# Kernel optimization log

Hardware: AMD Instinct MI355X
Metric: run time of the kernel (lower is better)

## Reference

```python
import jax, jax.numpy as jnp
import numpy as np

B, RATIO, IN_CH, H = 32, 32, 64, 8
E = IN_CH * H                 # embed_dim = in_channels * n_heads = 512
NODES_PER_GRAPH = 512
N = B * NODES_PER_GRAPH       # 16384 source nodes


def setup_inputs() -> dict:
    key = jax.random.key(0)
    ks = jax.random.split(key, 6)
    x = jax.random.normal(ks[0], (N, E), dtype=jnp.float32)
    # edge_index is accepted by forward but unused in 'attn' mode
    edge_index = jax.random.randint(ks[1], (2, 262144), 0, N, dtype=jnp.int32)
    # per-node graph id, sorted, equal-size graphs (batch[-1] + 1 == B)
    batch = jnp.repeat(jnp.arange(B, dtype=jnp.int32), NODES_PER_GRAPH)
    # learned params: cluster query seeds + MultiheadAttention in/out projections
    xcent_base = jax.random.normal(ks[2], (RATIO, E), dtype=jnp.float32)
    in_proj_w = jax.random.normal(ks[3], (3 * E, E), dtype=jnp.float32) / np.sqrt(E).astype(np.float32)
    in_proj_b = jnp.zeros((3 * E,), dtype=jnp.float32)
    out_proj_w = jax.random.normal(ks[4], (E, E), dtype=jnp.float32) / np.sqrt(E).astype(np.float32)
    out_proj_b = jnp.zeros((E,), dtype=jnp.float32)
    return dict(x=x, edge_index=edge_index, batch=batch, xcent_base=xcent_base,
                in_proj_w=in_proj_w, in_proj_b=in_proj_b,
                out_proj_w=out_proj_w, out_proj_b=out_proj_b)


def reference(x, edge_index, batch, xcent_base, in_proj_w, in_proj_b, out_proj_w, out_proj_b):
    # BipartPool.forward, mode='attn':
    #   x_aggrs = xcent_base.repeat(batch_size, 1)  -> queries [L, E], L = B*ratio
    #   MultiheadAttention(q=x_aggrs, k=v=x, attn_mask=mask[batch].T)
    # mask[batch].T is True (disallowed) where query's graph != node's graph.
    L = B * RATIO
    head_dim = E // H
    x_aggrs = jnp.tile(xcent_base, (B, 1))                        # [L, E]

    wq, wk, wv = jnp.split(in_proj_w, 3, axis=0)                  # each [E, E]
    bq, bk, bv = jnp.split(in_proj_b, 3, axis=0)
    q = (x_aggrs @ wq.T + bq).reshape(L, H, head_dim).transpose(1, 0, 2)  # [H, L, hd]
    k = (x @ wk.T + bk).reshape(N, H, head_dim).transpose(1, 0, 2)        # [H, N, hd]
    v = (x @ wv.T + bv).reshape(N, H, head_dim).transpose(1, 0, 2)        # [H, N, hd]

    batchcent = jnp.repeat(jnp.arange(B, dtype=batch.dtype), RATIO)       # [L]
    allowed = batchcent[:, None] == batch[None, :]                        # [L, N]

    scale = np.float32(1.0 / np.sqrt(head_dim))
    scores = jnp.einsum('hld,hnd->hln', q, k) * scale                     # [H, L, N]
    scores = jnp.where(allowed[None], scores, -jnp.inf)
    attn = jax.nn.softmax(scores, axis=-1)
    out = jnp.einsum('hln,hnd->hld', attn, v)                             # [H, L, hd]
    out = out.transpose(1, 0, 2).reshape(L, E)
    xcent = out @ out_proj_w.T + out_proj_b                               # [L, E]
    # original returns (xcent.reshape(B, ratio, E), None, None, batchcent, None, None)
    return xcent.reshape(B, RATIO, E), batchcent
```

## Files before the change

### kernel.cpp

```cpp
#include <hip/hip_runtime.h>
#include <hip/hip_bf16.h>

#define NGRAPH 32
#define NHEAD 8
#define EMB 512
#define NNODES 16384
#define NPG 512
#define LQ 1024
#define PST 520

typedef __attribute__((ext_vector_type(8))) short short8;
typedef __attribute__((ext_vector_type(4))) float f32x4;

static __device__ __forceinline__ unsigned short f2bf(float f) {
  union { float f; unsigned u; } v; v.f = f;
  unsigned r = (v.u + 0x7fffu + ((v.u >> 16) & 1u)) >> 16;
  return (unsigned short)r;
}

static __device__ __forceinline__ void gload_lds16(const ushort* g, ushort* l) {
  __builtin_amdgcn_global_load_lds(
      (const __attribute__((address_space(1))) unsigned*)g,
      (__attribute__((address_space(3))) unsigned*)l, 16, 0, 0);
}

#define BARRIER_LGKM()                                        \
  do {                                                        \
    asm volatile("s_waitcnt lgkmcnt(0)" ::: "memory");        \
    __builtin_amdgcn_s_barrier();                             \
  } while (0)

__global__ void prep_x(const float* __restrict__ x, ushort* __restrict__ xb,
                       ushort* __restrict__ xbT) {
  __shared__ ushort tile[32][33];
  int bc = blockIdx.x;
  int br = blockIdx.y;
  int t = threadIdx.x, lr = t >> 5, lc = t & 31;
#pragma unroll
  for (int p = 0; p < 4; ++p) {
    int r = lr + p * 8;
    long gi = (long)(br * 32 + r) * EMB + bc * 32 + lc;
    ushort b = f2bf(x[gi]);
    xb[gi] = b;
    tile[r][lc] = b;
  }
  __syncthreads();
#pragma unroll
  for (int p = 0; p < 4; ++p) {
    int r = lr + p * 8;
    xbT[(long)(bc * 32 + r) * NNODES + br * 32 + lc] = tile[lc][r];
  }
}

__global__ void prep_w(const float* __restrict__ wv, const float* __restrict__ wo,
                       const float* __restrict__ wq, const float* __restrict__ xc,
                       ushort* __restrict__ wvb, ushort* __restrict__ wob,
                       ushort* __restrict__ wqb, ushort* __restrict__ xcb,
                       float* __restrict__ bcent) {
  int b = blockIdx.x;
  if (b == 784) {
    int i = threadIdx.x;
#pragma unroll
    for (int p = 0; p < 4; ++p) bcent[i + p * 256] = (float)((i + p * 256) >> 5);
    return;
  }
  const float* src; ushort* dst; int off;
  if (b < 256)       { src = wv; dst = wvb; off = b; }
  else if (b < 512)  { src = wo; dst = wob; off = b - 256; }
  else if (b < 768)  { src = wq; dst = wqb; off = b - 512; }
  else               { src = xc; dst = xcb; off = b - 768; }
  int i = (off * 256 + threadIdx.x) * 4;
  float4 v = *reinterpret_cast<const float4*>(src + i);
  ushort4 o;
  o.x = f2bf(v.x); o.y = f2bf(v.y); o.z = f2bf(v.z); o.w = f2bf(v.w);
  *reinterpret_cast<ushort4*>(dst + i) = o;
}

__global__ void prep_wkT(const float* __restrict__ wk, ushort* __restrict__ wkT) {
  __shared__ ushort tile[32][33];
  int bd = blockIdx.x, bk = blockIdx.y;
  int t = threadIdx.x, lr = t >> 5, lc = t & 31;
#pragma unroll
  for (int p = 0; p < 4; ++p) {
    int r = lr + p * 8;
    tile[r][lc] = f2bf(0.125f * wk[(long)(bd * 32 + r) * EMB + bk * 32 + lc]);
  }
  __syncthreads();
#pragma unroll
  for (int p = 0; p < 4; ++p) {
    int r = lr + p * 8;
    wkT[(long)(bk * 32 + r) * EMB + bd * 32 + lc] = tile[lc][r];
  }
}

__global__ __launch_bounds__(256) void qpc_mfma(
    const ushort* __restrict__ xcb, const ushort* __restrict__ wqb,
    const float* __restrict__ bq, const ushort* __restrict__ wkTb,
    ushort* __restrict__ PCb) {
  __shared__ ushort Qs[32][72];
  int h = blockIdx.x >> 2, qs = blockIdx.x & 3;
  int t = threadIdx.x, w = t >> 6, lane = t & 63;
  int lr = lane & 15, grp = lane >> 4, ko = grp * 8;

  f32x4 qa[2];
  qa[0] = (f32x4)(0.0f); qa[1] = (f32x4)(0.0f);
#pragma unroll 4
  for (int kk = 0; kk < EMB; kk += 32) {
    short8 a0 = *reinterpret_cast<const short8*>(xcb + lr * EMB + kk + ko);
    short8 a1 = *reinterpret_cast<const short8*>(xcb + (16 + lr) * EMB + kk + ko);
    short8 b  = *reinterpret_cast<const short8*>(wqb + (long)(h * 64 + w * 16 + lr) * EMB + kk + ko);
    qa[0] = __builtin_amdgcn_mfma_f32_16x16x32_bf16(a0, b, qa[0], 0, 0, 0);
    qa[1] = __builtin_amdgcn_mfma_f32_16x16x32_bf16(a1, b, qa[1], 0, 0, 0);
  }
  float bias = bq[h * 64 + w * 16 + lr];
#pragma unroll
  for (int i = 0; i < 2; ++i)
#pragma unroll
    for (int r = 0; r < 4; ++r)
      Qs[i * 16 + grp * 4 + r][w * 16 + lr] = f2bf(qa[i][r] + bias);
  __syncthreads();

  f32x4 pa[2][2];
#pragma unroll
  for (int i = 0; i < 2; ++i)
#pragma unroll
    for (int j = 0; j < 2; ++j) pa[i][j] = (f32x4)(0.0f);
#pragma unroll
  for (int kk = 0; kk < 64; kk += 32) {
    short8 a0 = *reinterpret_cast<const short8*>(&Qs[lr][kk + ko]);
    short8 a1 = *reinterpret_cast<const short8*>(&Qs[16 + lr][kk + ko]);
#pragma unroll
    for (int j = 0; j < 2; ++j) {
      short8 b = *reinterpret_cast<const short8*>(
          wkTb + (long)(qs * 128 + w * 32 + j * 16 + lr) * EMB + h * 64 + kk + ko);
      pa[0][j] = __builtin_amdgcn_mfma_f32_16x16x32_bf16(a0, b, pa[0][j], 0, 0, 0);
      pa[1][j] = __builtin_amdgcn_mfma_f32_16x16x32_bf16(a1, b, pa[1][j], 0, 0, 0);
    }
  }
#pragma unroll
  for (int i = 0; i < 2; ++i)
#pragma unroll
    for (int j = 0; j < 2; ++j)
#pragma unroll
      for (int r = 0; r < 4; ++r)
        PCb[(long)(h * 32 + i * 16 + grp * 4 + r) * EMB + qs * 128 + w * 32 + j * 16 + lr] =
            f2bf(pa[i][j][r]);
}

__global__ __launch_bounds__(512, 2) void fused_attn(
    const ushort* __restrict__ PCb, const ushort* __restrict__ xb,
    const ushort* __restrict__ xbT, const ushort* __restrict__ wvb,
    const float* __restrict__ bvb, ushort* __restrict__ aout) {
  __shared__ ushort PCl[32 * PST];
  __shared__ ushort PBuf[32 * PST];
  __shared__ ushort Bbuf[2][16384];
  __shared__ float rmax[32][8];
  __shared__ float rsum[32][8];

  const int g = blockIdx.x & 31, h = blockIdx.x >> 5;
  const int t = threadIdx.x, w = t >> 6, lane = t & 63;
  const int lr = lane & 15, grp = lane >> 4;
  const int koU = grp * 8;

  const ushort* xg  = xb  + (long)g * NPG * EMB;
  const ushort* xTg = xbT + g * NPG;

  const int srow0 = w * 64 + (lane >> 2);
  const int spart = lane & 3;

  auto STAGE1 = [&](int c, int db) {
#pragma unroll
    for (int q = 0; q < 4; ++q) {
      int row = srow0 + q * 16;
      int psrc = spart ^ ((row >> 1) & 3);
      gload_lds16(xg + (long)row * EMB + c * 32 + psrc * 8,
                  &Bbuf[db][(w * 64 + q * 16) * 32]);
    }
  };
  auto STAGE3 = [&](int c, int db) {
#pragma unroll
    for (int q = 0; q < 4; ++q) {
      int row = srow0 + q * 16;
      int psrc = spart ^ ((row >> 1) & 3);
      gload_lds16(xTg + (long)row * NNODES + c * 32 + psrc * 8,
                  &Bbuf[db][(w * 64 + q * 16) * 32]);
    }
  };

  STAGE1(0, 0);
  STAGE1(1, 1);
  {
    const ushort* pc = PCb + h * 32 * EMB;
#pragma unroll
    for (int p = 0; p < 4; ++p) {
      int u = t + p * 512;
      int row = u >> 6, col = (u & 63) * 8;
      *reinterpret_cast<short8*>(&PCl[row * PST + col]) =
          *reinterpret_cast<const short8*>(pc + row * EMB + col);
    }
  }
  BARRIER_LGKM();

  f32x4 acc[2][4];
#pragma unroll
  for (int i = 0; i < 2; ++i)
#pragma unroll
    for (int j = 0; j < 4; ++j) acc[i][j] = (f32x4)(0.0f);

#pragma unroll
  for (int c = 0; c < 16; ++c) {
    const int db = c & 1;
    asm volatile("s_waitcnt vmcnt(4)" ::: "memory");
    __builtin_amdgcn_sched_barrier(0);
    short8 a0 = *reinterpret_cast<const short8*>(&PCl[lr * PST + c * 32 + koU]);
    short8 a1 = *reinterpret_cast<const short8*>(&PCl[(16 + lr) * PST + c * 32 + koU]);
    short8 bv[4];
#pragma unroll
    for (int j = 0; j < 4; ++j) {
      int n = w * 64 + j * 16 + lr;
      int psrc = grp ^ ((n >> 1) & 3);
      bv[j] = *reinterpret_cast<const short8*>(&Bbuf[db][n * 32 + psrc * 8]);
    }
#pragma unroll
    for (int j = 0; j < 4; ++j) {
      acc[0][j] = __builtin_amdgcn_mfma_f32_16x16x32_bf16(a0, bv[j], acc[0][j], 0, 0, 0);
      acc[1][j] = __builtin_amdgcn_mfma_f32_16x16x32_bf16(a1, bv[j], acc[1][j], 0, 0, 0);
    }
    __builtin_amdgcn_sched_barrier(0);
    if (c < 14) STAGE1(c + 2, db);
    else        STAGE3(c - 14, db);
  }

#pragma unroll
  for (int i = 0; i < 2; ++i)
#pragma unroll
    for (int r = 0; r < 4; ++r) {
      float m = fmaxf(fmaxf(acc[i][0][r], acc[i][1][r]), fmaxf(acc[i][2][r], acc[i][3][r]));
      m = fmaxf(m, __shfl_xor(m, 1)); m = fmaxf(m, __shfl_xor(m, 2));
      m = fmaxf(m, __shfl_xor(m, 4)); m = fmaxf(m, __shfl_xor(m, 8));
      if (lr == 0) rmax[i * 16 + grp * 4 + r][w] = m;
    }
  BARRIER_LGKM();
#pragma unroll
  for (int i = 0; i < 2; ++i)
#pragma unroll
    for (int r = 0; r < 4; ++r) {
      int row = i * 16 + grp * 4 + r;
      float m = rmax[row][0];
#pragma unroll
      for (int q = 1; q < 8; ++q) m = fmaxf(m, rmax[row][q]);
      float s = 0.f;
#pragma unroll
      for (int j = 0; j < 4; ++j) {
        float e = __expf(acc[i][j][r] - m);
        acc[i][j][r] = e;
        s += e;
      }
      s += __shfl_xor(s, 1); s += __shfl_xor(s, 2);
      s += __shfl_xor(s, 4); s += __shfl_xor(s, 8);
      if (lr == 0) rsum[row][w] = s;
    }
  BARRIER_LGKM();
#pragma unroll
  for (int i = 0; i < 2; ++i)
#pragma unroll
    for (int r = 0; r < 4; ++r) {
      int row = i * 16 + grp * 4 + r;
      float tot = rsum[row][0];
#pragma unroll
      for (int q = 1; q < 8; ++q) tot += rsum[row][q];
      float inv = 1.f / tot;
#pragma unroll
      for (int j = 0; j < 4; ++j)
        PBuf[row * PST + w * 64 + j * 16 + lr] = f2bf(acc[i][j][r] * inv);
    }
  BARRIER_LGKM();

  f32x4 acc2[2][4];
#pragma unroll
  for (int i = 0; i < 2; ++i)
#pragma unroll
    for (int j = 0; j < 4; ++j) acc2[i][j] = (f32x4)(0.0f);

#pragma unroll
  for (int c = 0; c < 16; ++c) {
    const int db = c & 1;
    if (c < 15) asm volatile("s_waitcnt vmcnt(4)" ::: "memory");
    else        asm volatile("s_waitcnt vmcnt(0)" ::: "memory");
    __builtin_amdgcn_sched_barrier(0);
    short8 a0 = *reinterpret_cast<const short8*>(&PBuf[lr * PST + c * 32 + koU]);
    short8 a1 = *reinterpret_cast<const short8*>(&PBuf[(16 + lr) * PST + c * 32 + koU]);
    short8 bv[4];
#pragma unroll
    for (int j = 0; j < 4; ++j) {
      int e = w * 64 + j * 16 + lr;
      int psrc = grp ^ ((e >> 1) & 3);
      bv[j] = *reinterpret_cast<const short8*>(&Bbuf[db][e * 32 + psrc * 8]);
    }
#pragma unroll
    for (int j = 0; j < 4; ++j) {
      acc2[0][j] = __builtin_amdgcn_mfma_f32_16x16x32_bf16(a0, bv[j], acc2[0][j], 0, 0, 0);
      acc2[1][j] = __builtin_amdgcn_mfma_f32_16x16x32_bf16(a1, bv[j], acc2[1][j], 0, 0, 0);
    }
    __builtin_amdgcn_sched_barrier(0);
    if (c < 14) STAGE3(c + 2, db);
  }
  BARRIER_LGKM();

#pragma unroll
  for (int i = 0; i < 2; ++i)
#pragma unroll
    for (int r = 0; r < 4; ++r) {
      int row = i * 16 + grp * 4 + r;
#pragma unroll
      for (int j = 0; j < 4; ++j)
        PBuf[row * PST + w * 64 + j * 16 + lr] = f2bf(acc2[i][j][r]);
    }
  BARRIER_LGKM();

  int wr = w >> 2, wc = w & 3;
  f32x4 acc3 = (f32x4)(0.0f);
  const ushort* wvh = wvb + (long)(h * 64 + wc * 16) * EMB;
#pragma unroll
  for (int c = 0; c < 16; ++c) {
    short8 a = *reinterpret_cast<const short8*>(&PBuf[(wr * 16 + lr) * PST + c * 32 + koU]);
    short8 b = *reinterpret_cast<const short8*>(wvh + (long)lr * EMB + c * 32 + koU);
    acc3 = __builtin_amdgcn_mfma_f32_16x16x32_bf16(a, b, acc3, 0, 0, 0);
  }
  float bias = bvb[h * 64 + wc * 16 + lr];
#pragma unroll
  for (int r = 0; r < 4; ++r) {
    int row = wr * 16 + grp * 4 + r;
    aout[(long)(g * 32 + row) * EMB + h * 64 + wc * 16 + lr] = f2bf(acc3[r] + bias);
  }
}

template <int KK, int FM, int FN, int WM, int WN, bool OUT_BF16, bool HAS_BIAS>
__global__ void gemm_abt(const ushort* __restrict__ A, const ushort* __restrict__ Bm,
                         void* __restrict__ C, const float* __restrict__ bias,
                         int lda, int ldb, int ldc) {
  int tid = threadIdx.x;
  int wave = tid >> 6, lane = tid & 63;
  int wr = wave / WN, wc = wave % WN;
  int rowBase = blockIdx.y * (WM * FM * 16) + wr * FM * 16;
  int colBase = blockIdx.x * (WN * FN * 16) + wc * FN * 16;
  int lr = lane & 15;
  int ko = (lane >> 4) * 8;

  f32x4 acc[FM][FN];
#pragma unroll
  for (int i = 0; i < FM; ++i)
#pragma unroll
    for (int j = 0; j < FN; ++j) acc[i][j] = (f32x4)(0.0f);

#pragma unroll 4
  for (int kk = 0; kk < KK; kk += 32) {
    short8 av[FM], bv[FN];
#pragma unroll
    for (int i = 0; i < FM; ++i)
      av[i] = *reinterpret_cast<const short8*>(A + (long)(rowBase + i * 16 + lr) * lda + kk + ko);
#pragma unroll
    for (int j = 0; j < FN; ++j)
      bv[j] = *reinterpret_cast<const short8*>(Bm + (long)(colBase + j * 16 + lr) * ldb + kk + ko);
#pragma unroll
    for (int i = 0; i < FM; ++i)
#pragma unroll
      for (int j = 0; j < FN; ++j)
        acc[i][j] = __builtin_amdgcn_mfma_f32_16x16x32_bf16(av[i], bv[j], acc[i][j], 0, 0, 0);
  }

  int or0 = (lane >> 4) * 4;
#pragma unroll
  for (int i = 0; i < FM; ++i) {
#pragma unroll
    for (int j = 0; j < FN; ++j) {
      int col = colBase + j * 16 + lr;
      float bval = HAS_BIAS ? bias[col] : 0.f;
#pragma unroll
      for (int r = 0; r < 4; ++r) {
        int row = rowBase + i * 16 + or0 + r;
        float v = acc[i][j][r] + bval;
        if (OUT_BF16)
          ((ushort*)C)[(long)row * ldc + col] = f2bf(v);
        else
          ((float*)C)[(long)row * ldc + col] = v;
      }
    }
  }
}

extern "C" void kernel_launch(void* const* d_in, const int* in_sizes, int n_in,
                              void* d_out, int out_size, void* d_ws, size_t ws_size,
                              hipStream_t stream) {
  const float* x          = (const float*)d_in[0];
  const float* xcent_base = (const float*)d_in[3];
  const float* in_proj_w  = (const float*)d_in[4];
  const float* in_proj_b  = (const float*)d_in[5];
  const float* out_proj_w = (const float*)d_in[6];
  const float* out_proj_b = (const float*)d_in[7];

  char* w = (char*)d_ws;
  ushort* xb   = (ushort*)(w);
  ushort* xbT  = (ushort*)(w + 16777216);
  ushort* PCb  = (ushort*)(w + 33554432);
  ushort* wvb  = (ushort*)(w + 33816576);
  ushort* wob  = (ushort*)(w + 34340864);
  ushort* wqb  = (ushort*)(w + 34865152);
  ushort* wkTb = (ushort*)(w + 35389440);
  ushort* xcb  = (ushort*)(w + 35913728);
  ushort* aout = (ushort*)(w + 35946496);

  const float* wq = in_proj_w;
  const float* wk = in_proj_w + 512 * 512;
  const float* wv = in_proj_w + 1024 * 512;
  const float* bq = in_proj_b;
  const float* bv = in_proj_b + 1024;

  prep_x<<<dim3(EMB / 32, NNODES / 32), 256, 0, stream>>>(x, xb, xbT);
  prep_w<<<785, 256, 0, stream>>>(wv, out_proj_w, wq, xcent_base,
                                  wvb, wob, wqb, xcb, (float*)d_out + LQ * EMB);
  prep_wkT<<<dim3(16, 16), 256, 0, stream>>>(wk, wkTb);
  qpc_mfma<<<32, 256, 0, stream>>>(xcb, wqb, bq, wkTb, PCb);

  fused_attn<<<256, 512, 0, stream>>>(PCb, xb, xbT, wvb, bv, aout);

  gemm_abt<512, 1, 2, 2, 2, false, true><<<dim3(8, 32, 1), 256, 0, stream>>>(
      aout, wob, d_out, out_proj_b, 512, 512, 512);
}
```

Baseline: 65.60 us.

## Widen attention blocks to 1024 threads, vectorize x prep, merge weight prep kernels

```diff
diff --git a/kernel.cpp b/kernel.cpp
--- a/kernel.cpp
+++ b/kernel.cpp
@@ -30,38 +30,69 @@
     __builtin_amdgcn_s_barrier();                             \
   } while (0)
 
-__global__ void prep_x(const float* __restrict__ x, ushort* __restrict__ xb,
-                       ushort* __restrict__ xbT) {
+__global__ __launch_bounds__(256) void prep_x(const float* __restrict__ x,
+                                              ushort* __restrict__ xb,
+                                              ushort* __restrict__ xbT) {
+  __shared__ ushort tile[64][68];
+  int id = blockIdx.x;
+  int xr = id & 7, j = id >> 3;
+  int m = j >> 6, r = j & 63;
+  int g = xr + 8 * m;
+  int bc = r & 7;
+  int br = g * 8 + (r >> 3);
+  int t = threadIdx.x;
+  int trr = t >> 4, tc = t & 15;
+#pragma unroll
+  for (int p = 0; p < 4; ++p) {
+    int n = trr + p * 16;
+    long gi = (long)(br * 64 + n) * EMB + bc * 64 + tc * 4;
+    float4 v = *reinterpret_cast<const float4*>(x + gi);
+    ushort4 o;
+    o.x = f2bf(v.x); o.y = f2bf(v.y); o.z = f2bf(v.z); o.w = f2bf(v.w);
+    *reinterpret_cast<ushort4*>(xb + gi) = o;
+    *reinterpret_cast<ushort4*>(&tile[n][tc * 4]) = o;
+  }
+  __syncthreads();
+#pragma unroll
+  for (int p = 0; p < 4; ++p) {
+    int e = trr + p * 16;
+    int n0 = tc * 4;
+    ushort4 o;
+    o.x = tile[n0][e]; o.y = tile[n0 + 1][e];
+    o.z = tile[n0 + 2][e]; o.w = tile[n0 + 3][e];
+    *reinterpret_cast<ushort4*>(xbT + (long)(bc * 64 + e) * NNODES + br * 64 + n0) = o;
+  }
+}
+
+__global__ void prep_wb(const float* __restrict__ wv, const float* __restrict__ wo,
+                        const float* __restrict__ wq, const float* __restrict__ xc,
+                        const float* __restrict__ wk,
+                        ushort* __restrict__ wvb, ushort* __restrict__ wob,
+                        ushort* __restrict__ wqb, ushort* __restrict__ xcb,
+                        ushort* __restrict__ wkT, float* __restrict__ bcent) {
   __shared__ ushort tile[32][33];
-  int bc = blockIdx.x;
-  int br = blockIdx.y;
-  int t = threadIdx.x, lr = t >> 5, lc = t & 31;
-#pragma unroll
-  for (int p = 0; p < 4; ++p) {
-    int r = lr + p * 8;
-    long gi = (long)(br * 32 + r) * EMB + bc * 32 + lc;
-    ushort b = f2bf(x[gi]);
-    xb[gi] = b;
-    tile[r][lc] = b;
-  }
-  __syncthreads();
-#pragma unroll
-  for (int p = 0; p < 4; ++p) {
-    int r = lr + p * 8;
-    xbT[(long)(bc * 32 + r) * NNODES + br * 32 + lc] = tile[lc][r];
-  }
-}
-
-__global__ void prep_w(const float* __restrict__ wv, const float* __restrict__ wo,
-                       const float* __restrict__ wq, const float* __restrict__ xc,
-                       ushort* __restrict__ wvb, ushort* __restrict__ wob,
-                       ushort* __restrict__ wqb, ushort* __restrict__ xcb,
-                       float* __restrict__ bcent) {
   int b = blockIdx.x;
   if (b == 784) {
     int i = threadIdx.x;
 #pragma unroll
     for (int p = 0; p < 4; ++p) bcent[i + p * 256] = (float)((i + p * 256) >> 5);
+    return;
+  }
+  if (b >= 785) {
+    int b2 = b - 785;
+    int bd = b2 >> 4, bk = b2 & 15;
+    int t = threadIdx.x, lr = t >> 5, lc = t & 31;
+#pragma unroll
+    for (int p = 0; p < 4; ++p) {
+      int rr = lr + p * 8;
+      tile[rr][lc] = f2bf(0.125f * wk[(long)(bd * 32 + rr) * EMB + bk * 32 + lc]);
+    }
+    __syncthreads();
+#pragma unroll
+    for (int p = 0; p < 4; ++p) {
+      int rr = lr + p * 8;
+      wkT[(long)(bk * 32 + rr) * EMB + bd * 32 + lc] = tile[lc][rr];
+    }
     return;
   }
   const float* src; ushort* dst; int off;
@@ -76,23 +107,6 @@
   *reinterpret_cast<ushort4*>(dst + i) = o;
 }
 
-__global__ void prep_wkT(const float* __restrict__ wk, ushort* __restrict__ wkT) {
-  __shared__ ushort tile[32][33];
-  int bd = blockIdx.x, bk = blockIdx.y;
-  int t = threadIdx.x, lr = t >> 5, lc = t & 31;
-#pragma unroll
-  for (int p = 0; p < 4; ++p) {
-    int r = lr + p * 8;
-    tile[r][lc] = f2bf(0.125f * wk[(long)(bd * 32 + r) * EMB + bk * 32 + lc]);
-  }
-  __syncthreads();
-#pragma unroll
-  for (int p = 0; p < 4; ++p) {
-    int r = lr + p * 8;
-    wkT[(long)(bk * 32 + r) * EMB + bd * 32 + lc] = tile[lc][r];
-  }
-}
-
 __global__ __launch_bounds__(256) void qpc_mfma(
     const ushort* __restrict__ xcb, const ushort* __restrict__ wqb,
     const float* __restrict__ bq, const ushort* __restrict__ wkTb,
@@ -147,15 +161,15 @@
             f2bf(pa[i][j][r]);
 }
 
-__global__ __launch_bounds__(512, 2) void fused_attn(
+__global__ __launch_bounds__(1024) void fused_attn(
     const ushort* __restrict__ PCb, const ushort* __restrict__ xb,
     const ushort* __restrict__ xbT, const ushort* __restrict__ wvb,
     const float* __restrict__ bvb, ushort* __restrict__ aout) {
   __shared__ ushort PCl[32 * PST];
   __shared__ ushort PBuf[32 * PST];
   __shared__ ushort Bbuf[2][16384];
-  __shared__ float rmax[32][8];
-  __shared__ float rsum[32][8];
+  __shared__ float rmax[32][16];
+  __shared__ float rsum[32][16];
 
   const int g = blockIdx.x & 31, h = blockIdx.x >> 5;
   const int t = threadIdx.x, w = t >> 6, lane = t & 63;
@@ -165,25 +179,25 @@
   const ushort* xg  = xb  + (long)g * NPG * EMB;
   const ushort* xTg = xbT + g * NPG;
 
-  const int srow0 = w * 64 + (lane >> 2);
+  const int srow0 = w * 32 + (lane >> 2);
   const int spart = lane & 3;
 
   auto STAGE1 = [&](int c, int db) {
 #pragma unroll
-    for (int q = 0; q < 4; ++q) {
+    for (int q = 0; q < 2; ++q) {
       int row = srow0 + q * 16;
       int psrc = spart ^ ((row >> 1) & 3);
       gload_lds16(xg + (long)row * EMB + c * 32 + psrc * 8,
-                  &Bbuf[db][(w * 64 + q * 16) * 32]);
+                  &Bbuf[db][(w * 32 + q * 16) * 32]);
     }
   };
   auto STAGE3 = [&](int c, int db) {
 #pragma unroll
-    for (int q = 0; q < 4; ++q) {
+    for (int q = 0; q < 2; ++q) {
       int row = srow0 + q * 16;
       int psrc = spart ^ ((row >> 1) & 3);
       gload_lds16(xTg + (long)row * NNODES + c * 32 + psrc * 8,
-                  &Bbuf[db][(w * 64 + q * 16) * 32]);
+                  &Bbuf[db][(w * 32 + q * 16) * 32]);
     }
   };
 
@@ -192,8 +206,8 @@
   {
     const ushort* pc = PCb + h * 32 * EMB;
 #pragma unroll
-    for (int p = 0; p < 4; ++p) {
-      int u = t + p * 512;
+    for (int p = 0; p < 2; ++p) {
+      int u = t + p * 1024;
       int row = u >> 6, col = (u & 63) * 8;
       *reinterpret_cast<short8*>(&PCl[row * PST + col]) =
           *reinterpret_cast<const short8*>(pc + row * EMB + col);
@@ -201,28 +215,28 @@
   }
   BARRIER_LGKM();
 
-  f32x4 acc[2][4];
-#pragma unroll
-  for (int i = 0; i < 2; ++i)
-#pragma unroll
-    for (int j = 0; j < 4; ++j) acc[i][j] = (f32x4)(0.0f);
+  f32x4 acc[2][2];
+#pragma unroll
+  for (int i = 0; i < 2; ++i)
+#pragma unroll
+    for (int j = 0; j < 2; ++j) acc[i][j] = (f32x4)(0.0f);
 
 #pragma unroll
   for (int c = 0; c < 16; ++c) {
     const int db = c & 1;
-    asm volatile("s_waitcnt vmcnt(4)" ::: "memory");
+    asm volatile("s_waitcnt vmcnt(2)" ::: "memory");
     __builtin_amdgcn_sched_barrier(0);
     short8 a0 = *reinterpret_cast<const short8*>(&PCl[lr * PST + c * 32 + koU]);
     short8 a1 = *reinterpret_cast<const short8*>(&PCl[(16 + lr) * PST + c * 32 + koU]);
-    short8 bv[4];
-#pragma unroll
-    for (int j = 0; j < 4; ++j) {
-      int n = w * 64 + j * 16 + lr;
+    short8 bv[2];
+#pragma unroll
+    for (int j = 0; j < 2; ++j) {
+      int n = w * 32 + j * 16 + lr;
       int psrc = grp ^ ((n >> 1) & 3);
       bv[j] = *reinterpret_cast<const short8*>(&Bbuf[db][n * 32 + psrc * 8]);
     }
 #pragma unroll
-    for (int j = 0; j < 4; ++j) {
+    for (int j = 0; j < 2; ++j) {
       acc[0][j] = __builtin_amdgcn_mfma_f32_16x16x32_bf16(a0, bv[j], acc[0][j], 0, 0, 0);
       acc[1][j] = __builtin_amdgcn_mfma_f32_16x16x32_bf16(a1, bv[j], acc[1][j], 0, 0, 0);
     }
@@ -235,7 +249,7 @@
   for (int i = 0; i < 2; ++i)
 #pragma unroll
     for (int r = 0; r < 4; ++r) {
-      float m = fmaxf(fmaxf(acc[i][0][r], acc[i][1][r]), fmaxf(acc[i][2][r], acc[i][3][r]));
+      float m = fmaxf(acc[i][0][r], acc[i][1][r]);
       m = fmaxf(m, __shfl_xor(m, 1)); m = fmaxf(m, __shfl_xor(m, 2));
       m = fmaxf(m, __shfl_xor(m, 4)); m = fmaxf(m, __shfl_xor(m, 8));
       if (lr == 0) rmax[i * 16 + grp * 4 + r][w] = m;
@@ -248,10 +262,10 @@
       int row = i * 16 + grp * 4 + r;
       float m = rmax[row][0];
 #pragma unroll
-      for (int q = 1; q < 8; ++q) m = fmaxf(m, rmax[row][q]);
+      for (int q = 1; q < 16; ++q) m = fmaxf(m, rmax[row][q]);
       float s = 0.f;
 #pragma unroll
-      for (int j = 0; j < 4; ++j) {
+      for (int j = 0; j < 2; ++j) {
         float e = __expf(acc[i][j][r] - m);
         acc[i][j][r] = e;
         s += e;
@@ -268,37 +282,37 @@
       int row = i * 16 + grp * 4 + r;
       float tot = rsum[row][0];
 #pragma unroll
-      for (int q = 1; q < 8; ++q) tot += rsum[row][q];
+      for (int q = 1; q < 16; ++q) tot += rsum[row][q];
       float inv = 1.f / tot;
 #pragma unroll
-      for (int j = 0; j < 4; ++j)
-        PBuf[row * PST + w * 64 + j * 16 + lr] = f2bf(acc[i][j][r] * inv);
-    }
-  BARRIER_LGKM();
-
-  f32x4 acc2[2][4];
-#pragma unroll
-  for (int i = 0; i < 2; ++i)
-#pragma unroll
-    for (int j = 0; j < 4; ++j) acc2[i][j] = (f32x4)(0.0f);
+      for (int j = 0; j < 2; ++j)
+        PBuf[row * PST + w * 32 + j * 16 + lr] = f2bf(acc[i][j][r] * inv);
+    }
+  BARRIER_LGKM();
+
+  f32x4 acc2[2][2];
+#pragma unroll
+  for (int i = 0; i < 2; ++i)
+#pragma unroll
+    for (int j = 0; j < 2; ++j) acc2[i][j] = (f32x4)(0.0f);
 
 #pragma unroll
   for (int c = 0; c < 16; ++c) {
     const int db = c & 1;
-    if (c < 15) asm volatile("s_waitcnt vmcnt(4)" ::: "memory");
+    if (c < 15) asm volatile("s_waitcnt vmcnt(2)" ::: "memory");
     else        asm volatile("s_waitcnt vmcnt(0)" ::: "memory");
     __builtin_amdgcn_sched_barrier(0);
     short8 a0 = *reinterpret_cast<const short8*>(&PBuf[lr * PST + c * 32 + koU]);
     short8 a1 = *reinterpret_cast<const short8*>(&PBuf[(16 + lr) * PST + c * 32 + koU]);
-    short8 bv[4];
-#pragma unroll
-    for (int j = 0; j < 4; ++j) {
-      int e = w * 64 + j * 16 + lr;
+    short8 bv[2];
+#pragma unroll
+    for (int j = 0; j < 2; ++j) {
+      int e = w * 32 + j * 16 + lr;
       int psrc = grp ^ ((e >> 1) & 3);
       bv[j] = *reinterpret_cast<const short8*>(&Bbuf[db][e * 32 + psrc * 8]);
     }
 #pragma unroll
-    for (int j = 0; j < 4; ++j) {
+    for (int j = 0; j < 2; ++j) {
       acc2[0][j] = __builtin_amdgcn_mfma_f32_16x16x32_bf16(a0, bv[j], acc2[0][j], 0, 0, 0);
       acc2[1][j] = __builtin_amdgcn_mfma_f32_16x16x32_bf16(a1, bv[j], acc2[1][j], 0, 0, 0);
     }
@@ -313,25 +327,27 @@
     for (int r = 0; r < 4; ++r) {
       int row = i * 16 + grp * 4 + r;
 #pragma unroll
-      for (int j = 0; j < 4; ++j)
-        PBuf[row * PST + w * 64 + j * 16 + lr] = f2bf(acc2[i][j][r]);
-    }
-  BARRIER_LGKM();
-
-  int wr = w >> 2, wc = w & 3;
-  f32x4 acc3 = (f32x4)(0.0f);
-  const ushort* wvh = wvb + (long)(h * 64 + wc * 16) * EMB;
-#pragma unroll
-  for (int c = 0; c < 16; ++c) {
-    short8 a = *reinterpret_cast<const short8*>(&PBuf[(wr * 16 + lr) * PST + c * 32 + koU]);
-    short8 b = *reinterpret_cast<const short8*>(wvh + (long)lr * EMB + c * 32 + koU);
-    acc3 = __builtin_amdgcn_mfma_f32_16x16x32_bf16(a, b, acc3, 0, 0, 0);
-  }
-  float bias = bvb[h * 64 + wc * 16 + lr];
-#pragma unroll
-  for (int r = 0; r < 4; ++r) {
-    int row = wr * 16 + grp * 4 + r;
-    aout[(long)(g * 32 + row) * EMB + h * 64 + wc * 16 + lr] = f2bf(acc3[r] + bias);
+      for (int j = 0; j < 2; ++j)
+        PBuf[row * PST + w * 32 + j * 16 + lr] = f2bf(acc2[i][j][r]);
+    }
+  BARRIER_LGKM();
+
+  if (w < 8) {
+    int wr = w >> 2, wc = w & 3;
+    f32x4 acc3 = (f32x4)(0.0f);
+    const ushort* wvh = wvb + (long)(h * 64 + wc * 16) * EMB;
+#pragma unroll
+    for (int c = 0; c < 16; ++c) {
+      short8 a = *reinterpret_cast<const short8*>(&PBuf[(wr * 16 + lr) * PST + c * 32 + koU]);
+      short8 b = *reinterpret_cast<const short8*>(wvh + (long)lr * EMB + c * 32 + koU);
+      acc3 = __builtin_amdgcn_mfma_f32_16x16x32_bf16(a, b, acc3, 0, 0, 0);
+    }
+    float bias = bvb[h * 64 + wc * 16 + lr];
+#pragma unroll
+    for (int r = 0; r < 4; ++r) {
+      int row = wr * 16 + grp * 4 + r;
+      aout[(long)(g * 32 + row) * EMB + h * 64 + wc * 16 + lr] = f2bf(acc3[r] + bias);
+    }
   }
 }
 
@@ -353,7 +369,7 @@
 #pragma unroll
     for (int j = 0; j < FN; ++j) acc[i][j] = (f32x4)(0.0f);
 
-#pragma unroll 4
+#pragma unroll 8
   for (int kk = 0; kk < KK; kk += 32) {
     short8 av[FM], bv[FN];
 #pragma unroll
@@ -416,13 +432,13 @@
   const float* bq = in_proj_b;
   const float* bv = in_proj_b + 1024;
 
-  prep_x<<<dim3(EMB / 32, NNODES / 32), 256, 0, stream>>>(x, xb, xbT);
-  prep_w<<<785, 256, 0, stream>>>(wv, out_proj_w, wq, xcent_base,
-                                  wvb, wob, wqb, xcb, (float*)d_out + LQ * EMB);
-  prep_wkT<<<dim3(16, 16), 256, 0, stream>>>(wk, wkTb);
+  prep_x<<<2048, 256, 0, stream>>>(x, xb, xbT);
+  prep_wb<<<1041, 256, 0, stream>>>(wv, out_proj_w, wq, xcent_base, wk,
+                                    wvb, wob, wqb, xcb, wkTb,
+                                    (float*)d_out + LQ * EMB);
   qpc_mfma<<<32, 256, 0, stream>>>(xcb, wqb, bq, wkTb, PCb);
 
-  fused_attn<<<256, 512, 0, stream>>>(PCb, xb, xbT, wvb, bv, aout);
+  fused_attn<<<256, 1024, 0, stream>>>(PCb, xb, xbT, wvb, bv, aout);
 
   gemm_abt<512, 1, 2, 2, 2, false, true><<<dim3(8, 32, 1), 256, 0, stream>>>(
       aout, wob, d_out, out_proj_b, 512, 512, 512);
```

Measured after the change: 62.94 us. 1.04x faster.
